# Performance work log

Measured on AMD Instinct MI355X. Metric: run time of the kernel, lower is better.

Reference implementation:

```python
import jax, jax.numpy as jnp
import numpy as np

H = 256
W = 256
N = 10000
CHUNK = 500  # N must be divisible by CHUNK
CHOL_BOUND = np.array([0.5, 0.0, 0.5], dtype=np.float32)  # cholesky_bound buffer


def setup_inputs() -> dict:
    key = jax.random.key(0)
    k1, k2, k3 = jax.random.split(key, 3)
    xyz = jax.random.normal(k1, (N, 2), dtype=jnp.float32)          # atanh-space positions
    cholesky = jax.random.uniform(k2, (N, 3), dtype=jnp.float32)    # lower-tri elems (pre-bound)
    colors = jax.random.normal(k3, (N, 3), dtype=jnp.float32)       # _colors (used raw)
    opacity = jnp.ones((N, 1), dtype=jnp.float32)                   # _opacity buffer
    scale_factor = jnp.asarray(1.0, dtype=jnp.float32)
    shift_factor = jnp.asarray(0.0, dtype=jnp.float32)
    return {"xyz": xyz, "cholesky": cholesky, "colors": colors,
            "opacity": opacity, "scale_factor": scale_factor, "shift_factor": shift_factor}


def _render(xyz, cholesky, colors, opacity, scale_factor, shift_factor):
    # --- project_gaussians_2d ---
    means = jnp.tanh(xyz)                                   # map to (-1, 1)
    cx = 0.5 * W * (means[:, 0] + 1.0)                      # pixel-space centers (N,)
    cy = 0.5 * H * (means[:, 1] + 1.0)
    L = cholesky + jnp.asarray(CHOL_BOUND)                  # get_cholesky_elements
    cov_xx = L[:, 0] * L[:, 0]
    cov_xy = L[:, 0] * L[:, 1]
    cov_yy = L[:, 1] * L[:, 1] + L[:, 2] * L[:, 2]
    det = cov_xx * cov_yy - cov_xy * cov_xy
    conic_a = cov_yy / det                                  # inverse covariance (conic)
    conic_b = -cov_xy / det
    conic_c = cov_xx / det
    op = opacity[:, 0]

    px = jnp.arange(W, dtype=jnp.float32)[None, :]          # (1, W) pixel x coords
    py = jnp.arange(H, dtype=jnp.float32)[:, None]          # (H, 1) pixel y coords

    def resh(v):
        return v.reshape((N // CHUNK, CHUNK) + v.shape[1:])

    stacked = jax.tree.map(resh, (cx, cy, conic_a, conic_b, conic_c, op, colors))

    # --- rasterize_gaussians_sum: out[h,w,:] = sum_n alpha_n(h,w) * color_n ---
    def body(acc, xs):
        cxc, cyc, ac, bc, cc, oc, colc = xs
        dx = cxc[:, None, None] - px[None]                  # (C, 1, W)
        dy = cyc[:, None, None] - py[None]                  # (C, H, 1)
        sigma = (0.5 * (ac[:, None, None] * dx * dx + cc[:, None, None] * dy * dy)
                 + bc[:, None, None] * (dx * dy))           # (C, H, W)
        alpha = oc[:, None, None] * jnp.exp(-sigma)
        alpha = jnp.where((sigma >= 0.0) & (alpha >= 1.0 / 255.0),
                          jnp.minimum(alpha, 0.999), 0.0)
        acc = acc + jnp.einsum('nhw,nc->hwc', alpha, colc)
        return acc, None

    img, _ = jax.lax.scan(body, jnp.zeros((H, W, 3), dtype=jnp.float32), stacked)
    img = img * scale_factor + shift_factor
    return jnp.transpose(img, (2, 0, 1))                    # (3, H, W)


def reference(xyz, cholesky, colors, opacity, scale_factor, shift_factor):
    return _render(xyz, cholesky, colors, opacity, scale_factor, shift_factor)
```

## Files before the change

### kernel.cpp

```cpp
#include <hip/hip_runtime.h>
#include <hip/hip_bf16.h>


#define IMG_H 256
#define IMG_W 256

__global__ __launch_bounds__(64) void splat_kernel(
    const float* __restrict__ xyz,
    const float* __restrict__ chol,
    const float* __restrict__ colors,
    const float* __restrict__ opacity,
    float* __restrict__ acc)
{
    const int n = blockIdx.x;

    const float mx = tanhf(xyz[2 * n + 0]);
    const float my = tanhf(xyz[2 * n + 1]);
    const float cx = 0.5f * IMG_W * (mx + 1.0f);
    const float cy = 0.5f * IMG_H * (my + 1.0f);

    const float L0 = chol[3 * n + 0] + 0.5f;
    const float L1 = chol[3 * n + 1] + 0.0f;
    const float L2 = chol[3 * n + 2] + 0.5f;
    const float cov_xx = L0 * L0;
    const float cov_xy = L0 * L1;
    const float cov_yy = L1 * L1 + L2 * L2;
    const float det = cov_xx * cov_yy - cov_xy * cov_xy;

    const float conic_a = cov_yy / det;
    const float conic_b = -cov_xy / det;
    const float conic_c = cov_xx / det;

    const float op = opacity[n];

    const float smax = logf(255.0f * op);
    if (!(smax > 0.0f)) return;

    const float rx = sqrtf(2.0f * smax * cov_xx) + 1.0f;
    const float ry = sqrtf(2.0f * smax * cov_yy) + 1.0f;
    const int x0 = max(0, (int)floorf(cx - rx));
    const int x1 = min(IMG_W - 1, (int)ceilf(cx + rx));
    const int y0 = max(0, (int)floorf(cy - ry));
    const int y1 = min(IMG_H - 1, (int)ceilf(cy + ry));
    if (x0 > x1 || y0 > y1) return;

    const int bw = x1 - x0 + 1;
    const int npix = bw * (y1 - y0 + 1);

    const float c0 = colors[3 * n + 0];
    const float c1 = colors[3 * n + 1];
    const float c2 = colors[3 * n + 2];

    for (int i = threadIdx.x; i < npix; i += 64) {
        const int yy = i / bw;
        const int xx = i - yy * bw;
        const float dx = cx - (float)(x0 + xx);
        const float dy = cy - (float)(y0 + yy);
        const float sigma =
            0.5f * (conic_a * dx * dx + conic_c * dy * dy) + conic_b * (dx * dy);
        float alpha = op * expf(-sigma);
        if (sigma >= 0.0f && alpha >= (1.0f / 255.0f)) {
            alpha = fminf(alpha, 0.999f);
            const int pix = (y0 + yy) * IMG_W + (x0 + xx);
            atomicAdd(&acc[0 * IMG_H * IMG_W + pix], alpha * c0);
            atomicAdd(&acc[1 * IMG_H * IMG_W + pix], alpha * c1);
            atomicAdd(&acc[2 * IMG_H * IMG_W + pix], alpha * c2);
        }
    }
}

__global__ __launch_bounds__(256) void finalize_kernel(
    const float* __restrict__ acc,
    const float* __restrict__ scale,
    const float* __restrict__ shift,
    float* __restrict__ out)
{
    const int i = blockIdx.x * 256 + threadIdx.x;
    if (i < 3 * IMG_H * IMG_W) {
        out[i] = acc[i] * scale[0] + shift[0];
    }
}

extern "C" void kernel_launch(void* const* d_in, const int* in_sizes, int n_in,
                              void* d_out, int out_size, void* d_ws, size_t ws_size,
                              hipStream_t stream) {
    const float* xyz     = (const float*)d_in[0];
    const float* chol    = (const float*)d_in[1];
    const float* colors  = (const float*)d_in[2];
    const float* opacity = (const float*)d_in[3];
    const float* scale   = (const float*)d_in[4];
    const float* shift   = (const float*)d_in[5];
    float* out = (float*)d_out;

    const int N = in_sizes[3];
    float* acc = (float*)d_ws;

    hipMemsetAsync(acc, 0, 3 * IMG_H * IMG_W * sizeof(float), stream);
    splat_kernel<<<N, 64, 0, stream>>>(xyz, chol, colors, opacity, acc);
    const int total = 3 * IMG_H * IMG_W;
    finalize_kernel<<<(total + 255) / 256, 256, 0, stream>>>(acc, scale, shift, out);
}
```

Baseline: 81.71 us.

## Replace atomic splatting with tile-binned gather rendering

```diff
diff --git a/kernel.cpp b/kernel.cpp
--- a/kernel.cpp
+++ b/kernel.cpp
@@ -1,18 +1,25 @@
 #include <hip/hip_runtime.h>
-#include <hip/hip_bf16.h>
 
 
 #define IMG_H 256
 #define IMG_W 256
+#define TILE 16
+#define TPX 16
+#define NTILES 256
+#define CAP 4096
 
-__global__ __launch_bounds__(64) void splat_kernel(
+__global__ __launch_bounds__(256) void prep_bin_kernel(
     const float* __restrict__ xyz,
     const float* __restrict__ chol,
     const float* __restrict__ colors,
     const float* __restrict__ opacity,
-    float* __restrict__ acc)
+    int N,
+    int* __restrict__ counts,
+    int* __restrict__ lists,
+    float4* __restrict__ params)
 {
-    const int n = blockIdx.x;
+    const int n = blockIdx.x * 256 + threadIdx.x;
+    if (n >= N) return;
 
     const float mx = tanhf(xyz[2 * n + 0]);
     const float my = tanhf(xyz[2 * n + 1]);
@@ -20,7 +27,7 @@
     const float cy = 0.5f * IMG_H * (my + 1.0f);
 
     const float L0 = chol[3 * n + 0] + 0.5f;
-    const float L1 = chol[3 * n + 1] + 0.0f;
+    const float L1 = chol[3 * n + 1];
     const float L2 = chol[3 * n + 2] + 0.5f;
     const float cov_xx = L0 * L0;
     const float cov_xy = L0 * L1;
@@ -30,8 +37,11 @@
     const float conic_a = cov_yy / det;
     const float conic_b = -cov_xy / det;
     const float conic_c = cov_xx / det;
+    const float op = opacity[n];
 
-    const float op = opacity[n];
+    params[3 * n + 0] = make_float4(cx, cy, conic_a, conic_b);
+    params[3 * n + 1] = make_float4(conic_c, op, colors[3 * n + 0], colors[3 * n + 1]);
+    params[3 * n + 2] = make_float4(colors[3 * n + 2], 0.0f, 0.0f, 0.0f);
 
     const float smax = logf(255.0f * op);
     if (!(smax > 0.0f)) return;
@@ -44,41 +54,73 @@
     const int y1 = min(IMG_H - 1, (int)ceilf(cy + ry));
     if (x0 > x1 || y0 > y1) return;
 
-    const int bw = x1 - x0 + 1;
-    const int npix = bw * (y1 - y0 + 1);
-
-    const float c0 = colors[3 * n + 0];
-    const float c1 = colors[3 * n + 1];
-    const float c2 = colors[3 * n + 2];
-
-    for (int i = threadIdx.x; i < npix; i += 64) {
-        const int yy = i / bw;
-        const int xx = i - yy * bw;
-        const float dx = cx - (float)(x0 + xx);
-        const float dy = cy - (float)(y0 + yy);
-        const float sigma =
-            0.5f * (conic_a * dx * dx + conic_c * dy * dy) + conic_b * (dx * dy);
-        float alpha = op * expf(-sigma);
-        if (sigma >= 0.0f && alpha >= (1.0f / 255.0f)) {
-            alpha = fminf(alpha, 0.999f);
-            const int pix = (y0 + yy) * IMG_W + (x0 + xx);
-            atomicAdd(&acc[0 * IMG_H * IMG_W + pix], alpha * c0);
-            atomicAdd(&acc[1 * IMG_H * IMG_W + pix], alpha * c1);
-            atomicAdd(&acc[2 * IMG_H * IMG_W + pix], alpha * c2);
+    const int tx0 = x0 >> 4, tx1 = x1 >> 4;
+    const int ty0 = y0 >> 4, ty1 = y1 >> 4;
+    for (int ty = ty0; ty <= ty1; ++ty) {
+        for (int tx = tx0; tx <= tx1; ++tx) {
+            const int t = ty * TPX + tx;
+            const int slot = atomicAdd(&counts[t], 1);
+            if (slot < CAP) lists[t * CAP + slot] = n;
         }
     }
 }
 
-__global__ __launch_bounds__(256) void finalize_kernel(
-    const float* __restrict__ acc,
+__global__ __launch_bounds__(256) void render_kernel(
+    const int* __restrict__ counts,
+    const int* __restrict__ lists,
+    const float4* __restrict__ params,
     const float* __restrict__ scale,
     const float* __restrict__ shift,
     float* __restrict__ out)
 {
-    const int i = blockIdx.x * 256 + threadIdx.x;
-    if (i < 3 * IMG_H * IMG_W) {
-        out[i] = acc[i] * scale[0] + shift[0];
+    const int tile = blockIdx.x;
+    const int tx = tile & (TPX - 1);
+    const int ty = tile >> 4;
+    const int lx = threadIdx.x & (TILE - 1);
+    const int ly = threadIdx.x >> 4;
+    const float px = (float)(tx * TILE + lx);
+    const float py = (float)(ty * TILE + ly);
+
+    __shared__ float4 sh[3 * 256];
+
+    const int cnt = min(counts[tile], CAP);
+    const int* list = lists + tile * CAP;
+
+    float accr = 0.0f, accg = 0.0f, accb = 0.0f;
+
+    for (int base = 0; base < cnt; base += 256) {
+        const int m = min(256, cnt - base);
+        __syncthreads();
+        if (threadIdx.x < m) {
+            const int n = list[base + threadIdx.x];
+            sh[3 * threadIdx.x + 0] = params[3 * n + 0];
+            sh[3 * threadIdx.x + 1] = params[3 * n + 1];
+            sh[3 * threadIdx.x + 2] = params[3 * n + 2];
+        }
+        __syncthreads();
+        for (int j = 0; j < m; ++j) {
+            const float4 p0 = sh[3 * j + 0];
+            const float4 p1 = sh[3 * j + 1];
+            const float c2v = sh[3 * j + 2].x;
+            const float dx = p0.x - px;
+            const float dy = p0.y - py;
+            const float sigma = 0.5f * (p0.z * dx * dx + p1.x * dy * dy) + p0.w * (dx * dy);
+            float alpha = p1.y * expf(-sigma);
+            if (sigma >= 0.0f && alpha >= (1.0f / 255.0f)) {
+                alpha = fminf(alpha, 0.999f);
+                accr = fmaf(alpha, p1.z, accr);
+                accg = fmaf(alpha, p1.w, accg);
+                accb = fmaf(alpha, c2v, accb);
+            }
+        }
     }
+
+    const float s = scale[0];
+    const float t = shift[0];
+    const int pix = (ty * TILE + ly) * IMG_W + (tx * TILE + lx);
+    out[0 * IMG_H * IMG_W + pix] = fmaf(accr, s, t);
+    out[1 * IMG_H * IMG_W + pix] = fmaf(accg, s, t);
+    out[2 * IMG_H * IMG_W + pix] = fmaf(accb, s, t);
 }
 
 extern "C" void kernel_launch(void* const* d_in, const int* in_sizes, int n_in,
@@ -93,10 +135,13 @@
     float* out = (float*)d_out;
 
     const int N = in_sizes[3];
-    float* acc = (float*)d_ws;
 
-    hipMemsetAsync(acc, 0, 3 * IMG_H * IMG_W * sizeof(float), stream);
-    splat_kernel<<<N, 64, 0, stream>>>(xyz, chol, colors, opacity, acc);
-    const int total = 3 * IMG_H * IMG_W;
-    finalize_kernel<<<(total + 255) / 256, 256, 0, stream>>>(acc, scale, shift, out);
+    int* counts = (int*)d_ws;
+    int* lists = counts + NTILES;
+    float4* params = (float4*)(lists + NTILES * CAP);
+
+    hipMemsetAsync(counts, 0, NTILES * sizeof(int), stream);
+    prep_bin_kernel<<<(N + 255) / 256, 256, 0, stream>>>(
+        xyz, chol, colors, opacity, N, counts, lists, params);
+    render_kernel<<<NTILES, 256, 0, stream>>>(counts, lists, params, scale, shift, out);
 }
```

Measured after the change: 100.1 us. +22.5%, slower.
